# Kernel tuning notes

Measured on AMD Instinct MI355X. Metric: run time of the kernel, lower is better.

Reference implementation:

```python
import jax, jax.numpy as jnp
import numpy as np

DIST_POWER = 1  # distance_power from init

def setup_inputs() -> dict:
    key = jax.random.key(0)
    k1, k2 = jax.random.split(key)
    N, D, C = 8192, 128, 256
    l_embeds = jax.random.normal(k1, (N, D), dtype=jnp.float32)
    l_labels = jax.random.randint(k2, (N,), 0, C, dtype=jnp.int64)
    return {"l_embeds": l_embeds, "l_labels": l_labels}

def reference(l_embeds, l_labels):
    # normalize_embeds=True
    x = l_embeds / jnp.linalg.norm(l_embeds, axis=1, keepdims=True)
    sq = jnp.sum(x * x, axis=1)  # [N]
    d2 = sq[:, None] + sq[None, :] - 2.0 * jnp.matmul(x, x.T)
    dist = jnp.sqrt(jnp.maximum(d2, 0.0))  # distance_power == 1
    if DIST_POWER != 1:
        dist = dist ** DIST_POWER
    N = x.shape[0]
    same = l_labels[:, None] == l_labels[None, :]
    eye = jnp.eye(N, dtype=bool)
    pos_mask = same & ~eye          # positives, diagonal removed (l is r)
    neg_mask = ~same
    # pos_dist = distmat * pos_mask (nan -> 0); hardest positive = argmax
    pos_dist = jnp.where(pos_mask, dist, 0.0)
    hardest_pos_inds = jnp.argmax(pos_dist, axis=1)
    # neg_dist = distmat with same-label entries set to +inf; hardest negative = argmin
    neg_dist = jnp.where(neg_mask, dist, jnp.inf)
    hardest_neg_inds = jnp.argmin(neg_dist, axis=1)
    anchor_inds = jnp.arange(N)
    # keep mask (all True by construction of labels); returned instead of
    # data-dependent boolean filtering to stay jit-compatible
    keep = jnp.any(pos_mask, axis=1) & jnp.any(neg_mask, axis=1)
    return anchor_inds, hardest_pos_inds, hardest_neg_inds, keep
```

## Files before the change

### kernel.cpp

```cpp
#include <hip/hip_runtime.h>
#include <math.h>

#define N 8192
#define D 128
#define C 256
#define CCAP 96
#define NT 64
#define NBLK (NT * (NT + 1) / 2)

typedef __attribute__((ext_vector_type(8))) short bf8;
typedef __attribute__((ext_vector_type(4))) float f4;

__device__ __forceinline__ unsigned short bf16_rtne(float f) {
    unsigned u = __float_as_uint(f);
    u += 0x7FFF + ((u >> 16) & 1);
    return (unsigned short)(u >> 16);
}
__device__ __forceinline__ float bf16_tof(unsigned short h) {
    return __uint_as_float((unsigned)h << 16);
}

__device__ __forceinline__ void async_cp16(const void* g, void* l) {
    __builtin_amdgcn_global_load_lds(
        (const __attribute__((address_space(1))) unsigned*)g,
        (__attribute__((address_space(3))) unsigned*)l, 16, 0, 0);
}

__device__ __forceinline__ unsigned int fbits(float f) {
    union { float f; unsigned int u; } x; x.f = f; return x.u;
}
__device__ __forceinline__ unsigned long long pack_pos(float v, int j) {
    return ((unsigned long long)fbits(v) << 32) | (unsigned int)(8191 - j);
}
__device__ __forceinline__ unsigned long long pack_neg(float v, int j) {
    return ((unsigned long long)fbits(v) << 32) | (unsigned int)j;
}
__device__ __forceinline__ void red_min(float& v, int& j, int mask) {
    const float ov = __shfl_xor(v, mask, 64);
    const int   oj = __shfl_xor(j, mask, 64);
    if (ov < v || (ov == v && oj < j)) { v = ov; j = oj; }
}

__global__ __launch_bounds__(256) void prep_kernel(
    const float* __restrict__ x, short* __restrict__ H,
    float* __restrict__ sq,
    unsigned long long* __restrict__ pos_pack,
    unsigned long long* __restrict__ neg_pack) {
    __shared__ float Xs[32 * 129];
    const int t = threadIdx.x;
    const int r0 = blockIdx.x * 32;

    if (t < 32) { pos_pack[r0 + t] = 0ULL; neg_pack[r0 + t] = ~0ULL; }

#pragma unroll
    for (int p = 0; p < 4; ++p) {
        const int lin = p * 256 + t;
        const int row = lin >> 5;
        const int c0 = (lin & 31) << 2;
        const float4 v = *(const float4*)(x + (size_t)(r0 + row) * D + c0);
        float* dst = &Xs[row * 129 + c0];
        dst[0] = v.x; dst[1] = v.y; dst[2] = v.z; dst[3] = v.w;
    }
    __syncthreads();

    const int r = t >> 3, q8 = t & 7;
    float* src = &Xs[r * 129 + q8 * 16];
    float s = 0.f;
#pragma unroll
    for (int i = 0; i < 16; ++i) s = fmaf(src[i], src[i], s);
    s += __shfl_xor(s, 1, 64);
    s += __shfl_xor(s, 2, 64);
    s += __shfl_xor(s, 4, 64);
    const float nrm = sqrtf(s);
    float t2 = 0.f;
#pragma unroll
    for (int i = 0; i < 16; ++i) {
        const float n = src[i] / nrm;
        src[i] = n;
        t2 = fmaf(n, n, t2);
    }
    t2 += __shfl_xor(t2, 1, 64);
    t2 += __shfl_xor(t2, 2, 64);
    t2 += __shfl_xor(t2, 4, 64);
    if (q8 == 0) sq[r0 + r] = t2;

    const size_t gbase = (size_t)(r0 + r) * D + q8 * 16;
#pragma unroll
    for (int g = 0; g < 4; ++g) {
        short4 o1, o2, o3;
        short* p1 = (short*)&o1; short* p2 = (short*)&o2; short* p3 = (short*)&o3;
#pragma unroll
        for (int i = 0; i < 4; ++i) {
            const float n = src[g * 4 + i];
            const unsigned short h1 = bf16_rtne(n);
            const float r1 = n - bf16_tof(h1);
            const unsigned short h2 = bf16_rtne(r1);
            const float r2 = r1 - bf16_tof(h2);
            const unsigned short h3 = bf16_rtne(r2);
            p1[i] = (short)h1; p2[i] = (short)h2; p3[i] = (short)h3;
        }
        *(short4*)(H + gbase + g * 4)                     = o1;
        *(short4*)(H + (size_t)N * D + gbase + g * 4)     = o2;
        *(short4*)(H + (size_t)2 * N * D + gbase + g * 4) = o3;
    }
}

__global__ __launch_bounds__(256) void posclass_kernel(
    const short* __restrict__ H, const float* __restrict__ sq,
    const int* __restrict__ labels,
    unsigned long long* __restrict__ pos_pack) {
    __shared__ float Xc[CCAP * 160];
    __shared__ float SqS[CCAP];
    __shared__ int   RwS[CCAP];
    __shared__ int   nS;
    const int c = blockIdx.x, t = threadIdx.x;
    const int k8 = t & 7;
    const int g  = t >> 3;

    if (t == 0) nS = 0;
    __syncthreads();
    for (int j = t; j < N; j += 256) {
        if (labels[j] == c) {
            const int s = atomicAdd(&nS, 1);
            if (s < CCAP) RwS[s] = j;
        }
    }
    __syncthreads();
    const int n = min(nS, CCAP);

    for (int lin = t; lin < n * 16; lin += 256) {
        const int i = lin >> 4, cc = lin & 15;
        const short* h0 = H + (size_t)RwS[i] * D + cc * 8;
        const bf8 L0 = *(const bf8*)h0;
        const bf8 L1 = *(const bf8*)(h0 + (size_t)N * D);
        const bf8 L2 = *(const bf8*)(h0 + (size_t)2 * N * D);
        float* dst = &Xc[i * 160 + (cc >> 1) * 20 + (cc & 1) * 8];
#pragma unroll
        for (int j = 0; j < 8; ++j)
            dst[j] = bf16_tof((unsigned short)L0[j])
                   + bf16_tof((unsigned short)L1[j])
                   + bf16_tof((unsigned short)L2[j]);
    }
    if (t < n) SqS[t] = sq[RwS[t]];
    __syncthreads();

    for (int i = g; i < n; i += 32) {
        float xi[16];
#pragma unroll
        for (int d = 0; d < 16; ++d) xi[d] = Xc[i * 160 + k8 * 20 + d];
        const float si = SqS[i];
        float best = -1.0f; int bestj = 0x7FFFFFFF;
        for (int j = 0; j < n; ++j) {
            if (j == i) continue;
            const float* xj = &Xc[j * 160 + k8 * 20];
            float p0 = 0.f, p1 = 0.f;
#pragma unroll
            for (int d = 0; d < 16; d += 2) {
                p0 = fmaf(xi[d],     xj[d],     p0);
                p1 = fmaf(xi[d + 1], xj[d + 1], p1);
            }
            float dot = p0 + p1;
            dot += __shfl_xor(dot, 1, 64);
            dot += __shfl_xor(dot, 2, 64);
            dot += __shfl_xor(dot, 4, 64);
            const float d2 = fmaxf(si + SqS[j] - 2.0f * dot, 0.0f);
            const int rj = RwS[j];
            if (d2 > best || (d2 == best && rj < bestj)) { best = d2; bestj = rj; }
        }
        if (k8 == 0)
            pos_pack[RwS[i]] = (best > 0.0f) ? pack_pos(best, bestj)
                                             : pack_pos(0.0f, 0);
    }
}

__global__ __launch_bounds__(256, 3) void miner_kernel(
    const short* __restrict__ H, const float* __restrict__ sq,
    const int* __restrict__ labels,
    unsigned long long* __restrict__ neg_pack) {
    __shared__ __align__(16) short sB[2 * 12288];
    __shared__ float sqS[256];
    __shared__ int   lbS[256];

    const int t = threadIdx.x;
    const int w = t >> 6;
    const int l = t & 63;
    const int quad = l >> 4;
    const int l16 = l & 15;

    const int b = blockIdx.x;
    int bi = (int)((129.0f - sqrtf(16641.0f - 8.0f * (float)b)) * 0.5f);
    while (bi > 0 && (bi * NT - bi * (bi - 1) / 2) > b) --bi;
    while (((bi + 1) * NT - (bi + 1) * bi / 2) <= b) ++bi;
    const int bj = bi + (b - (bi * NT - bi * (bi - 1) / 2));
    const int I0 = bi * 128, J0 = bj * 128;
    const bool diag = (bi == bj);

    float psq; int plb;
    {
        const int idx = ((t < 128) ? I0 : J0) + (t & 127);
        psq = sq[idx]; plb = labels[idx];
    }

    int gOffB[6], lOffB[6];
#pragma unroll
    for (int p = 0; p < 6; ++p) {
        const int limb = p >> 1;
        const int c2   = (p & 1) * 256 + t;
        const int smp  = c2 >> 2;
        const int sub  = c2 & 3;
        gOffB[p] = limb * (N * D) + (J0 + smp) * D + sub * 8;
        lOffB[p] = (limb * 128 + smp) * 32 + sub * 8;
    }
    int aGoff[3];
#pragma unroll
    for (int la = 0; la < 3; ++la)
        aGoff[la] = la * (N * D) + (I0 + w * 32 + l16) * D + quad * 8;

    f4 acc[2][8];
#pragma unroll
    for (int rt = 0; rt < 2; ++rt)
#pragma unroll
        for (int ct = 0; ct < 8; ++ct) acc[rt][ct] = (f4){0.f, 0.f, 0.f, 0.f};

    bf8 aF[2][3][2];
#pragma unroll
    for (int p = 0; p < 6; ++p)
        async_cp16(H + (size_t)gOffB[p], sB + lOffB[p]);
#pragma unroll
    for (int la = 0; la < 3; ++la)
#pragma unroll
        for (int rt = 0; rt < 2; ++rt)
            aF[0][la][rt] = *(const bf8*)(H + (size_t)(aGoff[la] + rt * 2048));

#pragma unroll
    for (int q = 0; q < 4; ++q) {
        const int cur = q & 1, nxt = cur ^ 1;
        const short* sBc = sB + cur * 12288;

        if (q < 3) {
            short* sBn = sB + nxt * 12288;
            const int kn = (q + 1) * 32;
#pragma unroll
            for (int p = 0; p < 6; ++p)
                async_cp16(H + (size_t)(gOffB[p] + kn), sBn + lOffB[p]);
#pragma unroll
            for (int la = 0; la < 3; ++la)
#pragma unroll
                for (int rt = 0; rt < 2; ++rt)
                    aF[nxt][la][rt] = *(const bf8*)
                        (H + (size_t)(aGoff[la] + rt * 2048 + kn));
            asm volatile("s_waitcnt vmcnt(12)" ::: "memory");
        } else {
            asm volatile("s_waitcnt vmcnt(0)" ::: "memory");
        }
        __builtin_amdgcn_s_barrier();
        __builtin_amdgcn_sched_barrier(0);

        __builtin_amdgcn_s_setprio(1);
#pragma unroll
        for (int ct = 0; ct < 8; ++ct) {
            bf8 bF[3];
#pragma unroll
            for (int lb = 0; lb < 3; ++lb)
                bF[lb] = *(const bf8*)
                    &sBc[(lb * 128 + ct * 16 + l16) * 32 + quad * 8];
#pragma unroll
            for (int rt = 0; rt < 2; ++rt) {
                acc[rt][ct] = __builtin_amdgcn_mfma_f32_16x16x32_bf16(
                    aF[cur][0][rt], bF[0], acc[rt][ct], 0, 0, 0);
                acc[rt][ct] = __builtin_amdgcn_mfma_f32_16x16x32_bf16(
                    aF[cur][0][rt], bF[1], acc[rt][ct], 0, 0, 0);
                acc[rt][ct] = __builtin_amdgcn_mfma_f32_16x16x32_bf16(
                    aF[cur][0][rt], bF[2], acc[rt][ct], 0, 0, 0);
                acc[rt][ct] = __builtin_amdgcn_mfma_f32_16x16x32_bf16(
                    aF[cur][1][rt], bF[0], acc[rt][ct], 0, 0, 0);
                acc[rt][ct] = __builtin_amdgcn_mfma_f32_16x16x32_bf16(
                    aF[cur][1][rt], bF[1], acc[rt][ct], 0, 0, 0);
                acc[rt][ct] = __builtin_amdgcn_mfma_f32_16x16x32_bf16(
                    aF[cur][2][rt], bF[0], acc[rt][ct], 0, 0, 0);
            }
        }
        __builtin_amdgcn_s_setprio(0);

        if (q < 2) {
            asm volatile("" ::: "memory");
            __builtin_amdgcn_s_barrier();
            __builtin_amdgcn_sched_barrier(0);
        }
    }

    sqS[t] = psq; lbS[t] = plb;
    __syncthreads();
    const float* sqI = sqS;       const float* sqJ = sqS + 128;
    const int*   lbI = lbS;       const int*   lbJ = lbS + 128;

    int ljv[8];
#pragma unroll
    for (int ct = 0; ct < 8; ++ct) ljv[ct] = lbJ[ct * 16 + l16];

    {
        float sjv[8];
#pragma unroll
        for (int ct = 0; ct < 8; ++ct) sjv[ct] = sqJ[ct * 16 + l16];
#pragma unroll
        for (int rt = 0; rt < 2; ++rt)
#pragma unroll
            for (int r = 0; r < 4; ++r) {
                const float si = sqI[w * 32 + rt * 16 + quad * 4 + r];
#pragma unroll
                for (int ct = 0; ct < 8; ++ct)
                    acc[rt][ct][r] =
                        fmaxf(si + sjv[ct] - 2.0f * acc[rt][ct][r], 0.0f);
            }
    }

#pragma unroll
    for (int rt = 0; rt < 2; ++rt)
#pragma unroll
        for (int r = 0; r < 4; ++r) {
            const int lr = w * 32 + rt * 16 + quad * 4 + r;
            const int liv = lbI[lr];
            float bnv = INFINITY; int bnj = 0;
#pragma unroll
            for (int ct = 0; ct < 8; ++ct) {
                const float vn = (liv == ljv[ct]) ? INFINITY : acc[rt][ct][r];
                const int col = J0 + ct * 16 + l16;
                if (vn < bnv) { bnv = vn; bnj = col; }
            }
            red_min(bnv, bnj, 1); red_min(bnv, bnj, 2);
            red_min(bnv, bnj, 4); red_min(bnv, bnj, 8);
            if (l16 == 0)
                atomicMin(&neg_pack[I0 + lr], pack_neg(bnv, bnj));
        }

    if (!diag) {
        unsigned long long* scr = (unsigned long long*)sB;
#pragma unroll
        for (int ct = 0; ct < 8; ++ct) {
            float bnv = INFINITY; int bnj = 0;
            const int lj = ljv[ct];
#pragma unroll
            for (int rt = 0; rt < 2; ++rt)
#pragma unroll
                for (int r = 0; r < 4; ++r) {
                    const int lr = w * 32 + rt * 16 + quad * 4 + r;
                    const float vn = (lbI[lr] == lj) ? INFINITY : acc[rt][ct][r];
                    if (vn < bnv) { bnv = vn; bnj = I0 + lr; }
                }
            red_min(bnv, bnj, 16); red_min(bnv, bnj, 32);
            if (quad == 0)
                scr[w * 128 + ct * 16 + l16] = pack_neg(bnv, bnj);
        }
        __syncthreads();
        if (t < 128) {
            unsigned long long mn = ~0ULL;
#pragma unroll
            for (int ww = 0; ww < 4; ++ww) {
                const unsigned long long qq = scr[ww * 128 + t];
                if (qq < mn) mn = qq;
            }
            atomicMin(&neg_pack[J0 + t], mn);
        }
    }
}

__global__ void finalize_kernel(const unsigned long long* __restrict__ pos_pack,
                                const unsigned long long* __restrict__ neg_pack,
                                int* __restrict__ out) {
    const int r = blockIdx.x * 256 + threadIdx.x;
    const unsigned long long pp = pos_pack[r];
    const unsigned long long np = neg_pack[r];
    out[r]         = r;
    out[N + r]     = 8191 - (int)(pp & 0xFFFFFFFFULL);
    out[2 * N + r] = (int)(np & 0xFFFFFFFFULL);
    out[3 * N + r] = (pp != 0ULL && np != ~0ULL) ? 1 : 0;
}

extern "C" void kernel_launch(void* const* d_in, const int* in_sizes, int n_in,
                              void* d_out, int out_size, void* d_ws, size_t ws_size,
                              hipStream_t stream) {
    const float* x      = (const float*)d_in[0];
    const int*   labels = (const int*)d_in[1];
    int* out = (int*)d_out;

    short* H = (short*)d_ws;
    float* sq = (float*)(H + (size_t)3 * N * D);
    unsigned long long* pos_pack =
        (unsigned long long*)(sq + N);
    unsigned long long* neg_pack = pos_pack + N;

    prep_kernel<<<N / 32, 256, 0, stream>>>(x, H, sq, pos_pack, neg_pack);
    posclass_kernel<<<C, 256, 0, stream>>>(H, sq, labels, pos_pack);
    miner_kernel<<<NBLK, 256, 0, stream>>>(H, sq, labels, neg_pack);
    finalize_kernel<<<N / 256, 256, 0, stream>>>(pos_pack, neg_pack, out);
}
```

Measured before the change: 163.1 us.

## Merge positive-class and negative-miner kernels into one launch sharing LDS via union

Combines the per-class positive search kernel and the tiled MFMA negative miner into a single launch, with the first C blocks doing the class work and the rest doing miner tiles. Shared memory is overlaid through a union so the miner's occupancy bound is kept. The class capacity is cut from 96 to 80 to fit the union within the miner's LDS budget. The aim is to remove a kernel boundary and let the class blocks overlap with the miner tiles. The risk is that classes with more than 80 members get truncated, which could give wrong positives.

```diff
diff --git a/kernel.cpp b/kernel.cpp
--- a/kernel.cpp
+++ b/kernel.cpp
@@ -4,7 +4,7 @@
 #define N 8192
 #define D 128
 #define C 256
-#define CCAP 96
+#define CCAP 80
 #define NT 64
 #define NBLK (NT * (NT + 1) / 2)
 
@@ -105,89 +105,98 @@
     }
 }
 
-__global__ __launch_bounds__(256) void posclass_kernel(
+union SMem {
+    struct {
+        short sB[2 * 12288];
+        float sqS[256];
+        int   lbS[256];
+    } m;
+    struct {
+        float Xc[CCAP * 160];
+        float Sq[CCAP];
+        int   Rw[CCAP];
+        int   n;
+    } p;
+};
+
+__global__ __launch_bounds__(256, 3) void fused_kernel(
     const short* __restrict__ H, const float* __restrict__ sq,
     const int* __restrict__ labels,
-    unsigned long long* __restrict__ pos_pack) {
-    __shared__ float Xc[CCAP * 160];
-    __shared__ float SqS[CCAP];
-    __shared__ int   RwS[CCAP];
-    __shared__ int   nS;
-    const int c = blockIdx.x, t = threadIdx.x;
-    const int k8 = t & 7;
-    const int g  = t >> 3;
-
-    if (t == 0) nS = 0;
-    __syncthreads();
-    for (int j = t; j < N; j += 256) {
-        if (labels[j] == c) {
-            const int s = atomicAdd(&nS, 1);
-            if (s < CCAP) RwS[s] = j;
-        }
-    }
-    __syncthreads();
-    const int n = min(nS, CCAP);
-
-    for (int lin = t; lin < n * 16; lin += 256) {
-        const int i = lin >> 4, cc = lin & 15;
-        const short* h0 = H + (size_t)RwS[i] * D + cc * 8;
-        const bf8 L0 = *(const bf8*)h0;
-        const bf8 L1 = *(const bf8*)(h0 + (size_t)N * D);
-        const bf8 L2 = *(const bf8*)(h0 + (size_t)2 * N * D);
-        float* dst = &Xc[i * 160 + (cc >> 1) * 20 + (cc & 1) * 8];
-#pragma unroll
-        for (int j = 0; j < 8; ++j)
-            dst[j] = bf16_tof((unsigned short)L0[j])
-                   + bf16_tof((unsigned short)L1[j])
-                   + bf16_tof((unsigned short)L2[j]);
-    }
-    if (t < n) SqS[t] = sq[RwS[t]];
-    __syncthreads();
-
-    for (int i = g; i < n; i += 32) {
-        float xi[16];
-#pragma unroll
-        for (int d = 0; d < 16; ++d) xi[d] = Xc[i * 160 + k8 * 20 + d];
-        const float si = SqS[i];
-        float best = -1.0f; int bestj = 0x7FFFFFFF;
-        for (int j = 0; j < n; ++j) {
-            if (j == i) continue;
-            const float* xj = &Xc[j * 160 + k8 * 20];
-            float p0 = 0.f, p1 = 0.f;
-#pragma unroll
-            for (int d = 0; d < 16; d += 2) {
-                p0 = fmaf(xi[d],     xj[d],     p0);
-                p1 = fmaf(xi[d + 1], xj[d + 1], p1);
-            }
-            float dot = p0 + p1;
-            dot += __shfl_xor(dot, 1, 64);
-            dot += __shfl_xor(dot, 2, 64);
-            dot += __shfl_xor(dot, 4, 64);
-            const float d2 = fmaxf(si + SqS[j] - 2.0f * dot, 0.0f);
-            const int rj = RwS[j];
-            if (d2 > best || (d2 == best && rj < bestj)) { best = d2; bestj = rj; }
-        }
-        if (k8 == 0)
-            pos_pack[RwS[i]] = (best > 0.0f) ? pack_pos(best, bestj)
-                                             : pack_pos(0.0f, 0);
-    }
-}
-
-__global__ __launch_bounds__(256, 3) void miner_kernel(
-    const short* __restrict__ H, const float* __restrict__ sq,
-    const int* __restrict__ labels,
+    unsigned long long* __restrict__ pos_pack,
     unsigned long long* __restrict__ neg_pack) {
-    __shared__ __align__(16) short sB[2 * 12288];
-    __shared__ float sqS[256];
-    __shared__ int   lbS[256];
-
+    __shared__ __align__(16) SMem sm;
     const int t = threadIdx.x;
+
+    if (blockIdx.x < C) {
+        const int c = blockIdx.x;
+        const int k8 = t & 7;
+        const int g  = t >> 3;
+
+        if (t == 0) sm.p.n = 0;
+        __syncthreads();
+        for (int j = t; j < N; j += 256) {
+            if (labels[j] == c) {
+                const int s = atomicAdd(&sm.p.n, 1);
+                if (s < CCAP) sm.p.Rw[s] = j;
+            }
+        }
+        __syncthreads();
+        const int n = min(sm.p.n, CCAP);
+
+        for (int lin = t; lin < n * 16; lin += 256) {
+            const int i = lin >> 4, cc = lin & 15;
+            const short* h0 = H + (size_t)sm.p.Rw[i] * D + cc * 8;
+            const bf8 L0 = *(const bf8*)h0;
+            const bf8 L1 = *(const bf8*)(h0 + (size_t)N * D);
+            const bf8 L2 = *(const bf8*)(h0 + (size_t)2 * N * D);
+            float* dst = &sm.p.Xc[i * 160 + (cc >> 1) * 20 + (cc & 1) * 8];
+#pragma unroll
+            for (int j = 0; j < 8; ++j)
+                dst[j] = bf16_tof((unsigned short)L0[j])
+                       + bf16_tof((unsigned short)L1[j])
+                       + bf16_tof((unsigned short)L2[j]);
+        }
+        if (t < n) sm.p.Sq[t] = sq[sm.p.Rw[t]];
+        __syncthreads();
+
+        for (int i = g; i < n; i += 32) {
+            float xi[16];
+#pragma unroll
+            for (int d = 0; d < 16; ++d) xi[d] = sm.p.Xc[i * 160 + k8 * 20 + d];
+            const float si = sm.p.Sq[i];
+            float best = -1.0f; int bestj = 0x7FFFFFFF;
+            for (int j = 0; j < n; ++j) {
+                if (j == i) continue;
+                const float* xj = &sm.p.Xc[j * 160 + k8 * 20];
+                float p0 = 0.f, p1 = 0.f;
+#pragma unroll
+                for (int d = 0; d < 16; d += 2) {
+                    p0 = fmaf(xi[d],     xj[d],     p0);
+                    p1 = fmaf(xi[d + 1], xj[d + 1], p1);
+                }
+                float dot = p0 + p1;
+                dot += __shfl_xor(dot, 1, 64);
+                dot += __shfl_xor(dot, 2, 64);
+                dot += __shfl_xor(dot, 4, 64);
+                const float d2 = fmaxf(si + sm.p.Sq[j] - 2.0f * dot, 0.0f);
+                const int rj = sm.p.Rw[j];
+                if (d2 > best || (d2 == best && rj < bestj)) {
+                    best = d2; bestj = rj;
+                }
+            }
+            if (k8 == 0)
+                pos_pack[sm.p.Rw[i]] = (best > 0.0f) ? pack_pos(best, bestj)
+                                                     : pack_pos(0.0f, 0);
+        }
+        return;
+    }
+
     const int w = t >> 6;
     const int l = t & 63;
     const int quad = l >> 4;
     const int l16 = l & 15;
 
-    const int b = blockIdx.x;
+    const int b = blockIdx.x - C;
     int bi = (int)((129.0f - sqrtf(16641.0f - 8.0f * (float)b)) * 0.5f);
     while (bi > 0 && (bi * NT - bi * (bi - 1) / 2) > b) --bi;
     while (((bi + 1) * NT - (bi + 1) * bi / 2) <= b) ++bi;
@@ -225,7 +234,7 @@
     bf8 aF[2][3][2];
 #pragma unroll
     for (int p = 0; p < 6; ++p)
-        async_cp16(H + (size_t)gOffB[p], sB + lOffB[p]);
+        async_cp16(H + (size_t)gOffB[p], sm.m.sB + lOffB[p]);
 #pragma unroll
     for (int la = 0; la < 3; ++la)
 #pragma unroll
@@ -235,10 +244,10 @@
 #pragma unroll
     for (int q = 0; q < 4; ++q) {
         const int cur = q & 1, nxt = cur ^ 1;
-        const short* sBc = sB + cur * 12288;
+        const short* sBc = sm.m.sB + cur * 12288;
 
         if (q < 3) {
-            short* sBn = sB + nxt * 12288;
+            short* sBn = sm.m.sB + nxt * 12288;
             const int kn = (q + 1) * 32;
 #pragma unroll
             for (int p = 0; p < 6; ++p)
@@ -289,10 +298,10 @@
         }
     }
 
-    sqS[t] = psq; lbS[t] = plb;
+    sm.m.sqS[t] = psq; sm.m.lbS[t] = plb;
     __syncthreads();
-    const float* sqI = sqS;       const float* sqJ = sqS + 128;
-    const int*   lbI = lbS;       const int*   lbJ = lbS + 128;
+    const float* sqI = sm.m.sqS;  const float* sqJ = sm.m.sqS + 128;
+    const int*   lbI = sm.m.lbS;  const int*   lbJ = sm.m.lbS + 128;
 
     int ljv[8];
 #pragma unroll
@@ -334,7 +343,7 @@
         }
 
     if (!diag) {
-        unsigned long long* scr = (unsigned long long*)sB;
+        unsigned long long* scr = (unsigned long long*)sm.m.sB;
 #pragma unroll
         for (int ct = 0; ct < 8; ++ct) {
             float bnv = INFINITY; int bnj = 0;
@@ -390,7 +399,7 @@
     unsigned long long* neg_pack = pos_pack + N;
 
     prep_kernel<<<N / 32, 256, 0, stream>>>(x, H, sq, pos_pack, neg_pack);
-    posclass_kernel<<<C, 256, 0, stream>>>(H, sq, labels, pos_pack);
-    miner_kernel<<<NBLK, 256, 0, stream>>>(H, sq, labels, neg_pack);
+    fused_kernel<<<C + NBLK, 256, 0, stream>>>(H, sq, labels, pos_pack,
+                                               neg_pack);
     finalize_kernel<<<N / 256, 256, 0, stream>>>(pos_pack, neg_pack, out);
 }
```

Result: faster. 136.9 us (-16.0%).
